# Kernel tuning notes

Hardware: AMD Instinct MI355X
Metric: run time of the kernel (lower is better)

## Reference

```python
import jax, jax.numpy as jnp
import numpy as np

N_NODES = 50000
N_EDGES = 800000
DIM = 128
HEADS = 2
DEPTH = 2
MLP = 512
NEG_SLOPE = 0.2  # PyG GATv2 default
EPS = 1e-5


def setup_inputs() -> dict:
    key = jax.random.key(0)
    ks = jax.random.split(key, 10)
    s = 0.05
    p = lambda k, shape: (jax.random.normal(k, shape, jnp.float32) * s)
    x = jax.random.normal(ks[0], (N_NODES, DIM), jnp.float32)
    edge_index = jax.random.randint(ks[1], (2, N_EDGES), 0, N_NODES, dtype=jnp.int64)
    D, H = DEPTH, HEADS
    return {
        "x": x,
        "edge_index": edge_index,
        # per-layer stacked params (leading dim = depth)
        "ln1_g": jnp.ones((D, DIM), jnp.float32), "ln1_b": jnp.zeros((D, DIM), jnp.float32),
        "Wl": p(ks[2], (D, DIM, H * DIM)), "bl": jnp.zeros((D, H * DIM), jnp.float32),
        "Wr": p(ks[3], (D, DIM, H * DIM)), "br": jnp.zeros((D, H * DIM), jnp.float32),
        "att": p(ks[4], (D, H, DIM)),
        "gat_b": jnp.zeros((D, H * DIM), jnp.float32),
        "proj_W": p(ks[5], (D, H * DIM, DIM)), "proj_b": jnp.zeros((D, DIM), jnp.float32),
        "ln2_g": jnp.ones((D, DIM), jnp.float32), "ln2_b": jnp.zeros((D, DIM), jnp.float32),
        "W1": p(ks[6], (D, DIM, MLP)), "b1": jnp.zeros((D, MLP), jnp.float32),
        "W2": p(ks[7], (D, MLP, DIM)), "b2": jnp.zeros((D, DIM), jnp.float32),
    }


def _layer_norm(x, g, b):
    m = jnp.mean(x, axis=-1, keepdims=True)
    v = jnp.var(x, axis=-1, keepdims=True)
    return (x - m) * jax.lax.rsqrt(v + EPS) * g + b


def _gatv2(x, src, dst, Wl, bl, Wr, br, att, gat_b):
    # GATv2Conv: e_ij = att^T LeakyReLU(Wl x_j + Wr x_i); alpha = segment-softmax over dst
    n = x.shape[0]
    xl = (x @ Wl + bl).reshape(n, HEADS, DIM)  # source transform [N,H,D]
    xr = (x @ Wr + br).reshape(n, HEADS, DIM)  # target transform [N,H,D]
    e = jax.nn.leaky_relu(xl[src] + xr[dst], NEG_SLOPE)      # [E,H,D]
    score = jnp.einsum('ehd,hd->eh', e, att)                 # [E,H]
    smax = jax.ops.segment_max(score, dst, num_segments=n)   # [N,H]
    ex = jnp.exp(score - smax[dst])
    denom = jax.ops.segment_sum(ex, dst, num_segments=n)     # [N,H]
    alpha = ex / (denom[dst] + 1e-16)                        # [E,H]
    msg = xl[src] * alpha[..., None]                         # [E,H,D]
    out = jax.ops.segment_sum(msg, dst, num_segments=n)      # [N,H,D]
    return out.reshape(n, HEADS * DIM) + gat_b


def reference(x, edge_index, ln1_g, ln1_b, Wl, bl, Wr, br, att, gat_b,
              proj_W, proj_b, ln2_g, ln2_b, W1, b1, W2, b2):
    src, dst = edge_index[0], edge_index[1]
    for i in range(DEPTH):
        h = _layer_norm(x, ln1_g[i], ln1_b[i])               # PreNorm
        g = _gatv2(h, src, dst, Wl[i], bl[i], Wr[i], br[i], att[i], gat_b[i])
        x = x + (g @ proj_W[i] + proj_b[i])                  # QuickFix proj + Residual
        h = _layer_norm(x, ln2_g[i], ln2_b[i])
        x = x + (jax.nn.gelu(h @ W1[i] + b1[i]) @ W2[i] + b2[i])  # FFN + Residual
    return x
```

## Files before the change

kernel.cpp:

```cpp
#include <hip/hip_runtime.h>

typedef unsigned int uint;
typedef unsigned short ushort;
typedef __attribute__((ext_vector_type(4))) float f32x4;
typedef __attribute__((ext_vector_type(2))) float f32x2;
typedef __attribute__((ext_vector_type(8))) short bf16x8;

#define N_NODES 50000
#define DIM 128
#define HEADS 2
#define HD 256
#define MLP 512
#define DEPTH 2
#define CAP 96

__device__ __forceinline__ uint f2bf(float f) {
    uint u = __float_as_uint(f);
    return (u + 0x7FFFu + ((u >> 16) & 1u)) >> 16;
}
__device__ __forceinline__ f32x2 bfpair(uint u) {
    f32x2 r;
    r.x = __uint_as_float(u << 16);
    r.y = __uint_as_float(u & 0xFFFF0000u);
    return r;
}

__device__ __forceinline__ float gelu_tanh(float x) {
    float t = 0.7978845608028654f * (x + 0.044715f * x * x * x);
    float e = __expf(2.0f * t);
    float th = 1.0f - 2.0f / (e + 1.0f);
    return 0.5f * x * (1.0f + th);
}

__global__ __launch_bounds__(256) void ln_kernel(
    const float* __restrict__ x, const float* __restrict__ g,
    const float* __restrict__ b, ushort* __restrict__ out, int N)
{
    int node = blockIdx.x * 4 + (threadIdx.x >> 6);
    if (node >= N) return;
    int lane = threadIdx.x & 63;
    const float2 v = *(const float2*)(x + (size_t)node * DIM + lane * 2);
    float s = v.x + v.y;
    float s2 = v.x * v.x + v.y * v.y;
    #pragma unroll
    for (int m = 1; m <= 32; m <<= 1) {
        s  += __shfl_xor(s,  m, 64);
        s2 += __shfl_xor(s2, m, 64);
    }
    float mean = s * (1.0f / 128.0f);
    float var  = s2 * (1.0f / 128.0f) - mean * mean;
    float rs = rsqrtf(var + 1e-5f);
    float ox = (v.x - mean) * rs * g[lane * 2]     + b[lane * 2];
    float oy = (v.y - mean) * rs * g[lane * 2 + 1] + b[lane * 2 + 1];
    uint pk = f2bf(ox) | (f2bf(oy) << 16);
    *(uint*)(out + (size_t)node * DIM + lane * 2) = pk;
}

__global__ __launch_bounds__(256) void wconv_all(
    const float* __restrict__ Wl, const float* __restrict__ Wr,
    const float* __restrict__ pW, const float* __restrict__ W1,
    const float* __restrict__ W2, ushort* __restrict__ WlWr_t,
    ushort* __restrict__ pW_t, ushort* __restrict__ W1_t,
    ushort* __restrict__ W2_t)
{
    int i = blockIdx.x * 256 + threadIdx.x;
    if (i < 65536) {
        int l = i >> 15, rem = i & 32767;
        int k = rem >> 8, m = rem & 255;
        WlWr_t[l * 65536 + m * 128 + k] = (ushort)f2bf(Wl[i]);
    } else if (i < 131072) {
        int j = i - 65536;
        int l = j >> 15, rem = j & 32767;
        int k = rem >> 8, m = rem & 255;
        WlWr_t[l * 65536 + (m + 256) * 128 + k] = (ushort)f2bf(Wr[j]);
    } else if (i < 196608) {
        int j = i - 131072;
        int l = j >> 15, rem = j & 32767;
        int k = rem >> 7, m = rem & 127;
        pW_t[l * 32768 + m * 256 + k] = (ushort)f2bf(pW[j]);
    } else if (i < 327680) {
        int j = i - 196608;
        int l = j >> 16, rem = j & 65535;
        int k = rem >> 9, m = rem & 511;
        W1_t[l * 65536 + m * 128 + k] = (ushort)f2bf(W1[j]);
    } else if (i < 458752) {
        int j = i - 327680;
        int l = j >> 16, rem = j & 65535;
        int k = rem >> 7, m = rem & 127;
        W2_t[l * 65536 + m * 512 + k] = (ushort)f2bf(W2[j]);
    }
}

template<int EPI>
__global__ __launch_bounds__(256) void gemm_mfma(
    const ushort* __restrict__ A, const ushort* __restrict__ Bt,
    const float* __restrict__ bias, const float* __restrict__ bias2, int bsplit,
    const float* __restrict__ R, void* __restrict__ Cout, int Nr, int K, int M)
{
    __shared__ ushort As[128 * 72];
    __shared__ ushort Bs[64 * 72];
    const int tid = threadIdx.x;
    const int wave = tid >> 6, lane = tid & 63;
    const int wm = wave >> 1, wn = wave & 1;
    const int r0 = blockIdx.y * 128;
    const int c0 = blockIdx.x * 64;
    const int l15 = lane & 15, q = lane >> 4;

    f32x4 acc[4][2];
    #pragma unroll
    for (int t = 0; t < 4; ++t)
        #pragma unroll
        for (int u = 0; u < 2; ++u) {
            f32x4 z = {0.f, 0.f, 0.f, 0.f};
            acc[t][u] = z;
        }

    for (int k0 = 0; k0 < K; k0 += 64) {
        #pragma unroll
        for (int p = 0; p < 4; ++p) {
            int flat = p * 256 + tid;
            int row = flat >> 3, c8 = flat & 7;
            int gr = r0 + row; gr = gr < Nr ? gr : Nr - 1;
            uint4 v = *(const uint4*)(A + (size_t)gr * K + k0 + c8 * 8);
            *(uint4*)(As + row * 72 + c8 * 8) = v;
        }
        #pragma unroll
        for (int p = 0; p < 2; ++p) {
            int flat = p * 256 + tid;
            int row = flat >> 3, c8 = flat & 7;
            uint4 v = *(const uint4*)(Bt + (size_t)(c0 + row) * K + k0 + c8 * 8);
            *(uint4*)(Bs + row * 72 + c8 * 8) = v;
        }
        __syncthreads();
        #pragma unroll
        for (int kh = 0; kh < 2; ++kh) {
            const int ko = kh * 32 + q * 8;
            bf16x8 a[4], b[2];
            #pragma unroll
            for (int t = 0; t < 4; ++t)
                a[t] = *(const bf16x8*)(As + (wm * 64 + t * 16 + l15) * 72 + ko);
            #pragma unroll
            for (int u = 0; u < 2; ++u)
                b[u] = *(const bf16x8*)(Bs + (wn * 32 + u * 16 + l15) * 72 + ko);
            #pragma unroll
            for (int t = 0; t < 4; ++t)
                #pragma unroll
                for (int u = 0; u < 2; ++u)
                    acc[t][u] = __builtin_amdgcn_mfma_f32_16x16x32_bf16(
                        a[t], b[u], acc[t][u], 0, 0, 0);
        }
        __syncthreads();
    }

    #pragma unroll
    for (int t = 0; t < 4; ++t) {
        int grow = r0 + wm * 64 + t * 16 + q * 4;
        #pragma unroll
        for (int u = 0; u < 2; ++u) {
            int gcol = c0 + wn * 32 + u * 16 + l15;
            float bv = (gcol < bsplit) ? bias[gcol] : bias2[gcol - bsplit];
            #pragma unroll
            for (int i = 0; i < 4; ++i) {
                int r = grow + i;
                if (r >= Nr) continue;
                float v = acc[t][u][i] + bv;
                if (EPI == 1) v = gelu_tanh(v);
                if (EPI == 2) {
                    v += R[(size_t)r * M + gcol];
                    ((float*)Cout)[(size_t)r * M + gcol] = v;
                } else {
                    ((ushort*)Cout)[(size_t)r * M + gcol] = (ushort)f2bf(v);
                }
            }
        }
    }
}

__global__ __launch_bounds__(256) void bucket_kernel(
    const int* __restrict__ src, const int* __restrict__ dst,
    int* __restrict__ deg, ushort* __restrict__ esrc, int E)
{
    int e = blockIdx.x * 256 + threadIdx.x;
    if (e >= E) return;
    int d = dst[e];
    int pos = atomicAdd(&deg[d], 1);
    if (pos < CAP) esrc[(size_t)d * CAP + pos] = (ushort)src[e];
}

__global__ __launch_bounds__(256) void gat_gather(
    const int* __restrict__ deg, const ushort* __restrict__ esrc,
    const ushort* __restrict__ xlr, const float* __restrict__ att,
    const float* __restrict__ gat_b, ushort* __restrict__ agg, int N)
{
    int node = blockIdx.x * 4 + (threadIdx.x >> 6);
    if (node >= N) return;
    const int lane = threadIdx.x & 63;
    const int half = lane >> 5, sl = lane & 31;
    const int c = sl * 8;

    const uint4 rq = *(const uint4*)(xlr + (size_t)node * 512 + 256 + c);
    const f32x2 r01 = bfpair(rq.x), r23 = bfpair(rq.y);
    const f32x2 r45 = bfpair(rq.z), r67 = bfpair(rq.w);
    const float4 af0 = *(const float4*)(att + c);
    const float4 af1 = *(const float4*)(att + c + 4);
    const f32x2 a01 = {af0.x, af0.y}, a23 = {af0.z, af0.w};
    const f32x2 a45 = {af1.x, af1.y}, a67 = {af1.z, af1.w};

    int dc = deg[node]; dc = dc < CAP ? dc : CAP;
    const int base = node * CAP;
    f32x2 acc01 = {0.f, 0.f}, acc23 = {0.f, 0.f}, acc45 = {0.f, 0.f}, acc67 = {0.f, 0.f};
    float den = 0.f;

    if (dc > 0) {
        int slc = sl < dc ? sl : dc - 1;
        const int idxreg = esrc[base + slc];

        auto getsrc = [&](int e) -> int {
            int idx = e < dc ? e : dc - 1;
            int s = __shfl(idxreg, (lane & 32) | (idx & 31), 64);
            if (idx >= 32) s = esrc[base + idx];
            return s;
        };

        const int iters = (dc + 1) >> 1;
        int e0 = half;
        int s0 = getsrc(e0);
        uint4 lq0 = *(const uint4*)(xlr + (size_t)s0 * 512 + c);
        int e1 = e0 + 2;
        int s1 = getsrc(e1);
        uint4 lq1 = *(const uint4*)(xlr + (size_t)s1 * 512 + c);

        for (int it = 0; it < iters; ++it) {
            const int e2 = e0 + 4;
            const int s2 = getsrc(e2);
            const uint4 lq2 = *(const uint4*)(xlr + (size_t)s2 * 512 + c);

            const f32x2 l01 = bfpair(lq0.x), l23 = bfpair(lq0.y);
            const f32x2 l45 = bfpair(lq0.z), l67 = bfpair(lq0.w);
            f32x2 t, p2;
            t = l01 + r01; p2  = a01 * __builtin_elementwise_max(t, 0.2f * t);
            t = l23 + r23; p2 += a23 * __builtin_elementwise_max(t, 0.2f * t);
            t = l45 + r45; p2 += a45 * __builtin_elementwise_max(t, 0.2f * t);
            t = l67 + r67; p2 += a67 * __builtin_elementwise_max(t, 0.2f * t);
            float p = p2.x + p2.y;
            p += __shfl_xor(p, 1, 64);
            p += __shfl_xor(p, 2, 64);
            p += __shfl_xor(p, 4, 64);
            p += __shfl_xor(p, 8, 64);
            const float ex = (e0 < dc) ? __expf(p) : 0.f;
            acc01 += ex * l01; acc23 += ex * l23; acc45 += ex * l45; acc67 += ex * l67;
            den += ex;
            e0 = e1; lq0 = lq1;
            e1 = e2; lq1 = lq2;
        }
    }
    acc01.x += __shfl_xor(acc01.x, 32, 64); acc01.y += __shfl_xor(acc01.y, 32, 64);
    acc23.x += __shfl_xor(acc23.x, 32, 64); acc23.y += __shfl_xor(acc23.y, 32, 64);
    acc45.x += __shfl_xor(acc45.x, 32, 64); acc45.y += __shfl_xor(acc45.y, 32, 64);
    acc67.x += __shfl_xor(acc67.x, 32, 64); acc67.y += __shfl_xor(acc67.y, 32, 64);
    den     += __shfl_xor(den,     32, 64);

    if (half == 0) {
        const float inv = 1.0f / (den + 1e-16f);
        const float4 g0 = *(const float4*)(gat_b + c);
        const float4 g1 = *(const float4*)(gat_b + c + 4);
        uint4 o;
        o.x = f2bf(acc01.x * inv + g0.x) | (f2bf(acc01.y * inv + g0.y) << 16);
        o.y = f2bf(acc23.x * inv + g0.z) | (f2bf(acc23.y * inv + g0.w) << 16);
        o.z = f2bf(acc45.x * inv + g1.x) | (f2bf(acc45.y * inv + g1.y) << 16);
        o.w = f2bf(acc67.x * inv + g1.z) | (f2bf(acc67.y * inv + g1.w) << 16);
        *(uint4*)(agg + (size_t)node * HD + c) = o;
    }
}

extern "C" void kernel_launch(void* const* d_in, const int* in_sizes, int n_in,
                              void* d_out, int out_size, void* d_ws, size_t ws_size,
                              hipStream_t stream) {
    const float* x_in   = (const float*)d_in[0];
    const int*   eidx   = (const int*)d_in[1];
    const float* ln1_g  = (const float*)d_in[2];
    const float* ln1_b  = (const float*)d_in[3];
    const float* Wl     = (const float*)d_in[4];
    const float* bl     = (const float*)d_in[5];
    const float* Wr     = (const float*)d_in[6];
    const float* br     = (const float*)d_in[7];
    const float* att    = (const float*)d_in[8];
    const float* gat_b  = (const float*)d_in[9];
    const float* projW  = (const float*)d_in[10];
    const float* projb  = (const float*)d_in[11];
    const float* ln2_g  = (const float*)d_in[12];
    const float* ln2_b  = (const float*)d_in[13];
    const float* W1     = (const float*)d_in[14];
    const float* b1     = (const float*)d_in[15];
    const float* W2     = (const float*)d_in[16];
    const float* b2     = (const float*)d_in[17];

    const int N = N_NODES;
    const int E = in_sizes[1] / 2;
    const int* src = eidx;
    const int* dst = eidx + E;

    char* ws = (char*)d_ws;
    size_t off = 0;
    ushort* xlr  = (ushort*)(ws + off); off += (size_t)N * 512 * 2;
    ushort* agg  = (ushort*)(ws + off); off += (size_t)N * HD * 2;
    ushort* h    = (ushort*)(ws + off); off += (size_t)N * DIM * 2;
    ushort* WlWr_t = (ushort*)(ws + off); off += (size_t)DEPTH * 512 * 128 * 2;
    ushort* pW_t   = (ushort*)(ws + off); off += (size_t)DEPTH * 128 * 256 * 2;
    ushort* W1_t   = (ushort*)(ws + off); off += (size_t)DEPTH * 512 * 128 * 2;
    ushort* W2_t   = (ushort*)(ws + off); off += (size_t)DEPTH * 128 * 512 * 2;
    int* deg     = (int*)(ws + off);    off += (size_t)N * 4;
    ushort* esrc = (ushort*)(ws + off); off += (size_t)N * CAP * 2;
    ushort* mid  = xlr;

    float* x = (float*)d_out;

    const int nodeBlocks = (N + 3) / 4;
    const dim3 blk(256);
    const int gy = (N + 127) / 128;

    wconv_all<<<(458752 + 255) / 256, blk, 0, stream>>>(
        Wl, Wr, projW, W1, W2, WlWr_t, pW_t, W1_t, W2_t);

    hipMemsetAsync(deg, 0, (size_t)N * 4, stream);
    bucket_kernel<<<(E + 255) / 256, blk, 0, stream>>>(src, dst, deg, esrc, E);

    for (int L = 0; L < DEPTH; ++L) {
        const float* bl_i   = bl + (size_t)L * HD;
        const float* br_i   = br + (size_t)L * HD;
        const float* att_i  = att + (size_t)L * HD;
        const float* gatb_i = gat_b + (size_t)L * HD;
        const float* pb_i   = projb + (size_t)L * DIM;
        const float* b1_i   = b1 + (size_t)L * MLP;
        const float* b2_i   = b2 + (size_t)L * DIM;
        const float* xin_L  = (L == 0) ? x_in : x;

        ln_kernel<<<nodeBlocks, blk, 0, stream>>>(xin_L, ln1_g + L * DIM, ln1_b + L * DIM, h, N);
        gemm_mfma<0><<<dim3(8, gy), blk, 0, stream>>>(
            h, WlWr_t + (size_t)L * 512 * 128, bl_i, br_i, HD, nullptr, xlr, N, 128, 512);
        gat_gather<<<nodeBlocks, blk, 0, stream>>>(deg, esrc, xlr, att_i, gatb_i, agg, N);
        gemm_mfma<2><<<dim3(2, gy), blk, 0, stream>>>(
            agg, pW_t + (size_t)L * 128 * 256, pb_i, pb_i, 1 << 30, xin_L, x, N, 256, 128);
        ln_kernel<<<nodeBlocks, blk, 0, stream>>>(x, ln2_g + L * DIM, ln2_b + L * DIM, h, N);
        gemm_mfma<1><<<dim3(8, gy), blk, 0, stream>>>(
            h, W1_t + (size_t)L * 512 * 128, b1_i, b1_i, 1 << 30, nullptr, mid, N, 128, 512);
        gemm_mfma<2><<<dim3(2, gy), blk, 0, stream>>>(
            mid, W2_t + (size_t)L * 128 * 512, b2_i, b2_i, 1 << 30, x, x, N, 512, 128);
    }
}
```

Measured before the change: 555.5 us.

## Store GATv2 node transforms in fp16 and score edges with packed fdot2

The Wl/Wr GEMM epilogue (EPI 0) now writes fp16 instead of bf16, and the edge gather computes the LeakyReLU attention score with packed half math and v_dot2 instructions. The attention vector is prescaled by log2(e) so exp2 can be used. Source-index fetching moves from a shuffle-based register cache to direct loads with a deeper prefetch of the next index, and the loop is unrolled by 2. This cuts ALU work in the gather loop at the cost of fp16 range and precision in the scores and features, and adds an extra memory load per edge for the index.

```diff
diff --git a/kernel.cpp b/kernel.cpp
--- a/kernel.cpp
+++ b/kernel.cpp
@@ -5,6 +5,7 @@
 typedef __attribute__((ext_vector_type(4))) float f32x4;
 typedef __attribute__((ext_vector_type(2))) float f32x2;
 typedef __attribute__((ext_vector_type(8))) short bf16x8;
+typedef _Float16 f16x2 __attribute__((ext_vector_type(2)));
 
 #define N_NODES 50000
 #define DIM 128
@@ -18,12 +19,27 @@
     uint u = __float_as_uint(f);
     return (u + 0x7FFFu + ((u >> 16) & 1u)) >> 16;
 }
-__device__ __forceinline__ f32x2 bfpair(uint u) {
-    f32x2 r;
-    r.x = __uint_as_float(u << 16);
-    r.y = __uint_as_float(u & 0xFFFF0000u);
-    return r;
-}
+__device__ __forceinline__ ushort f2h(float f) {
+    union { _Float16 h; ushort u; } v;
+    v.h = (_Float16)f;
+    return v.u;
+}
+__device__ __forceinline__ f16x2 u2h(uint u) {
+    union { uint u; f16x2 h; } v;
+    v.u = u;
+    return v.h;
+}
+
+#if __has_builtin(__builtin_amdgcn_fdot2)
+#define FDOT2(a, b, c) __builtin_amdgcn_fdot2((a), (b), (c), false)
+#else
+#define FDOT2(a, b, c) fmaf((float)(a)[0], (float)(b)[0], fmaf((float)(a)[1], (float)(b)[1], (c)))
+#endif
+#if __has_builtin(__builtin_amdgcn_exp2f)
+#define EXP2F(x) __builtin_amdgcn_exp2f(x)
+#else
+#define EXP2F(x) exp2f(x)
+#endif
 
 __device__ __forceinline__ float gelu_tanh(float x) {
     float t = 0.7978845608028654f * (x + 0.044715f * x * x * x);
@@ -168,6 +184,8 @@
                 if (EPI == 2) {
                     v += R[(size_t)r * M + gcol];
                     ((float*)Cout)[(size_t)r * M + gcol] = v;
+                } else if (EPI == 0) {
+                    ((ushort*)Cout)[(size_t)r * M + gcol] = f2h(v);
                 } else {
                     ((ushort*)Cout)[(size_t)r * M + gcol] = (ushort)f2bf(v);
                 }
@@ -199,59 +217,70 @@
     const int c = sl * 8;
 
     const uint4 rq = *(const uint4*)(xlr + (size_t)node * 512 + 256 + c);
-    const f32x2 r01 = bfpair(rq.x), r23 = bfpair(rq.y);
-    const f32x2 r45 = bfpair(rq.z), r67 = bfpair(rq.w);
+    const f16x2 r01 = u2h(rq.x), r23 = u2h(rq.y);
+    const f16x2 r45 = u2h(rq.z), r67 = u2h(rq.w);
+
+    const float LOG2E = 1.4426950408889634f;
     const float4 af0 = *(const float4*)(att + c);
     const float4 af1 = *(const float4*)(att + c + 4);
-    const f32x2 a01 = {af0.x, af0.y}, a23 = {af0.z, af0.w};
-    const f32x2 a45 = {af1.x, af1.y}, a67 = {af1.z, af1.w};
+    f16x2 a01, a23, a45, a67;
+    a01[0] = (_Float16)(af0.x * LOG2E); a01[1] = (_Float16)(af0.y * LOG2E);
+    a23[0] = (_Float16)(af0.z * LOG2E); a23[1] = (_Float16)(af0.w * LOG2E);
+    a45[0] = (_Float16)(af1.x * LOG2E); a45[1] = (_Float16)(af1.y * LOG2E);
+    a67[0] = (_Float16)(af1.z * LOG2E); a67[1] = (_Float16)(af1.w * LOG2E);
+    const f16x2 k02 = { (_Float16)0.2f, (_Float16)0.2f };
 
     int dc = deg[node]; dc = dc < CAP ? dc : CAP;
-    const int base = node * CAP;
+    const ushort* eb = esrc + node * CAP;
     f32x2 acc01 = {0.f, 0.f}, acc23 = {0.f, 0.f}, acc45 = {0.f, 0.f}, acc67 = {0.f, 0.f};
     float den = 0.f;
 
     if (dc > 0) {
-        int slc = sl < dc ? sl : dc - 1;
-        const int idxreg = esrc[base + slc];
-
-        auto getsrc = [&](int e) -> int {
-            int idx = e < dc ? e : dc - 1;
-            int s = __shfl(idxreg, (lane & 32) | (idx & 31), 64);
-            if (idx >= 32) s = esrc[base + idx];
-            return s;
+        const int dcm1 = dc - 1;
+        auto ldsrc = [&](int e) -> int {
+            int i = e < dc ? e : dcm1;
+            return (int)eb[i];
         };
-
+        auto ldrow = [&](int s) -> uint4 {
+            return *(const uint4*)(xlr + (size_t)s * 512 + c);
+        };
+
+        int e0 = half;
+        int s2 = ldsrc(e0 + 4);
+        uint4 lq0 = ldrow(ldsrc(e0));
+        uint4 lq1 = ldrow(ldsrc(e0 + 2));
         const int iters = (dc + 1) >> 1;
-        int e0 = half;
-        int s0 = getsrc(e0);
-        uint4 lq0 = *(const uint4*)(xlr + (size_t)s0 * 512 + c);
-        int e1 = e0 + 2;
-        int s1 = getsrc(e1);
-        uint4 lq1 = *(const uint4*)(xlr + (size_t)s1 * 512 + c);
-
+
+        #pragma unroll 2
         for (int it = 0; it < iters; ++it) {
-            const int e2 = e0 + 4;
-            const int s2 = getsrc(e2);
-            const uint4 lq2 = *(const uint4*)(xlr + (size_t)s2 * 512 + c);
-
-            const f32x2 l01 = bfpair(lq0.x), l23 = bfpair(lq0.y);
-            const f32x2 l45 = bfpair(lq0.z), l67 = bfpair(lq0.w);
-            f32x2 t, p2;
-            t = l01 + r01; p2  = a01 * __builtin_elementwise_max(t, 0.2f * t);
-            t = l23 + r23; p2 += a23 * __builtin_elementwise_max(t, 0.2f * t);
-            t = l45 + r45; p2 += a45 * __builtin_elementwise_max(t, 0.2f * t);
-            t = l67 + r67; p2 += a67 * __builtin_elementwise_max(t, 0.2f * t);
-            float p = p2.x + p2.y;
+            const int s3 = ldsrc(e0 + 6);
+            const uint4 lq2 = ldrow(s2);
+
+            const f16x2 l01 = u2h(lq0.x), l23 = u2h(lq0.y);
+            const f16x2 l45 = u2h(lq0.z), l67 = u2h(lq0.w);
+            f16x2 t, lr;
+            float p = 0.f;
+            t = l01 + r01; lr = __builtin_elementwise_max(t, t * k02); p = FDOT2(a01, lr, p);
+            t = l23 + r23; lr = __builtin_elementwise_max(t, t * k02); p = FDOT2(a23, lr, p);
+            t = l45 + r45; lr = __builtin_elementwise_max(t, t * k02); p = FDOT2(a45, lr, p);
+            t = l67 + r67; lr = __builtin_elementwise_max(t, t * k02); p = FDOT2(a67, lr, p);
             p += __shfl_xor(p, 1, 64);
             p += __shfl_xor(p, 2, 64);
             p += __shfl_xor(p, 4, 64);
             p += __shfl_xor(p, 8, 64);
-            const float ex = (e0 < dc) ? __expf(p) : 0.f;
-            acc01 += ex * l01; acc23 += ex * l23; acc45 += ex * l45; acc67 += ex * l67;
+            const float ex = (e0 < dc) ? EXP2F(p) : 0.f;
+            acc01.x = fmaf(ex, (float)l01[0], acc01.x);
+            acc01.y = fmaf(ex, (float)l01[1], acc01.y);
+            acc23.x = fmaf(ex, (float)l23[0], acc23.x);
+            acc23.y = fmaf(ex, (float)l23[1], acc23.y);
+            acc45.x = fmaf(ex, (float)l45[0], acc45.x);
+            acc45.y = fmaf(ex, (float)l45[1], acc45.y);
+            acc67.x = fmaf(ex, (float)l67[0], acc67.x);
+            acc67.y = fmaf(ex, (float)l67[1], acc67.y);
             den += ex;
-            e0 = e1; lq0 = lq1;
-            e1 = e2; lq1 = lq2;
+            e0 += 2;
+            s2 = s3;
+            lq0 = lq1; lq1 = lq2;
         }
     }
     acc01.x += __shfl_xor(acc01.x, 32, 64); acc01.y += __shfl_xor(acc01.y, 32, 64);
```

Result: slower. 577.8 us (+4.0%).
